# Kernel tuning notes

Measured on AMD Instinct MI355X. Metric: run time of the kernel, lower is better.

Reference implementation:

```python
import jax, jax.numpy as jnp
import numpy as np
from jax import lax

NODATA_VALUE = 0.0
RADIUS = 16  # structuring element size = 2*RADIUS + 1 = 33


def setup_inputs() -> dict:
    key = jax.random.key(0)
    # binary-ish raster: ~half pixels equal the nodata value (0.0)
    x = jax.random.randint(key, (8, 2048, 2048, 1), 0, 2).astype(jnp.float32)
    return {"x": x}


def reference(x):
    # nodata mask: 1 where x == nodata, else 0 (uint8 in original; float here for reduce_window)
    mask = jnp.where(jnp.equal(x, NODATA_VALUE), 1.0, 0.0).astype(x.dtype)
    se = 1 + 2 * RADIUS
    # tf.nn.dilation2d with an all-zeros kernel == sliding-window max over (se x se),
    # SAME padding. A square max window is separable: row-max then column-max.
    m = lax.reduce_window(mask, -jnp.inf, lax.max,
                          window_dimensions=(1, se, 1, 1),
                          window_strides=(1, 1, 1, 1),
                          padding="SAME")
    m = lax.reduce_window(m, -jnp.inf, lax.max,
                          window_dimensions=(1, 1, se, 1),
                          window_strides=(1, 1, 1, 1),
                          padding="SAME")
    return m.astype(jnp.uint8)
```

## Files before the change

### kernel.cpp

```cpp
#include <hip/hip_runtime.h>
#include <stdint.h>


#define HH_ 2048
#define WW_PX 2048
#define WW 32
#define RAD 16
#define ROWS 16
#define TPB2 512

typedef float  vfloat4 __attribute__((ext_vector_type(4)));
typedef int    vint4   __attribute__((ext_vector_type(4)));

__device__ __forceinline__ uint64_t spread4(uint64_t x) {
  x &= 0xFFFFULL;
  x = (x | (x << 24)) & 0x000000FF000000FFULL;
  x = (x | (x << 12)) & 0x000F000F000F000FULL;
  x = (x | (x << 6))  & 0x0303030303030303ULL;
  x = (x | (x << 3))  & 0x1111111111111111ULL;
  return x;
}

__global__ __launch_bounds__(256) void pack_kernel(const float* __restrict__ x,
                                                   uint64_t* __restrict__ packed) {
  const long long px0 = ((long long)blockIdx.x * 256 + threadIdx.x) * 4;
  const vfloat4 v = __builtin_nontemporal_load((const vfloat4*)(x + px0));
  const unsigned long long m0 = __ballot(v.x == 0.0f);
  const unsigned long long m1 = __ballot(v.y == 0.0f);
  const unsigned long long m2 = __ballot(v.z == 0.0f);
  const unsigned long long m3 = __ballot(v.w == 0.0f);
  const int lane = threadIdx.x & 63;
  if ((lane & 15) == 0) {
    const int sh = lane;
    uint64_t w = spread4(m0 >> sh)
               | (spread4(m1 >> sh) << 1)
               | (spread4(m2 >> sh) << 2)
               | (spread4(m3 >> sh) << 3);
    packed[px0 >> 6] = w;
  }
}

__global__ __launch_bounds__(TPB2) void dilate_kernel(const uint64_t* __restrict__ packed,
                                                      int* __restrict__ out) {
  __shared__ uint64_t stage[ROWS + 2 * RAD][WW];
  __shared__ uint64_t vall[ROWS][WW + 2];
  __shared__ uint64_t hrow[ROWS][WW];

  const int t = threadIdx.x;
  const int gr0 = blockIdx.x * ROWS;
  const int n = gr0 >> 11;
  const int h0 = gr0 & 2047;
  const uint64_t* base = packed + (long long)n * (HH_ * WW);

#pragma unroll
  for (int i = 0; i < (ROWS + 2 * RAD) * WW / TPB2; ++i) {
    const int idx = i * TPB2 + t;
    const int rr = idx >> 5;
    const int w_ = idx & 31;
    int hh = h0 + rr - RAD;
    hh = hh < 0 ? 0 : (hh > HH_ - 1 ? HH_ - 1 : hh);
    stage[rr][w_] = base[hh * WW + w_];
  }
  __syncthreads();

  const int w = t & 31;
  const int r = t >> 5;
  uint64_t v = 0;
#pragma unroll
  for (int i = 0; i <= 2 * RAD; ++i) v |= stage[r + i][w];
  vall[r][w + 1] = v;
  if (w == 0) { vall[r][0] = 0; vall[r][WW + 1] = 0; }
  __syncthreads();

  {
    const uint64_t p = vall[r][w];
    const uint64_t c = vall[r][w + 1];
    const uint64_t nx = vall[r][w + 2];
    uint64_t res = c;
#pragma unroll
    for (int s = 1; s <= RAD; ++s) {
      res |= (c >> s) | (nx << (64 - s));
      res |= (c << s) | (p >> (64 - s));
    }
    hrow[r][w] = res;
  }
  __syncthreads();

  int* obase = out + (long long)gr0 * WW_PX;
#pragma unroll
  for (int it = 0; it < 16; ++it) {
    const int f = it * TPB2 + t;
    const int row_l = f >> 9;
    const int wi = (f >> 4) & 31;
    const int sh = (f & 15) * 4;
    const uint64_t bits = hrow[row_l][wi] >> sh;
    vint4 o;
    o.x = (int)(bits & 1);
    o.y = (int)((bits >> 1) & 1);
    o.z = (int)((bits >> 2) & 1);
    o.w = (int)((bits >> 3) & 1);
    __builtin_nontemporal_store(o, (vint4*)(obase + (long long)f * 4));
  }
}

extern "C" void kernel_launch(void* const* d_in, const int* in_sizes, int n_in,
                              void* d_out, int out_size, void* d_ws, size_t ws_size,
                              hipStream_t stream) {
  const float* x = (const float*)d_in[0];
  int* out = (int*)d_out;
  uint64_t* packed = (uint64_t*)d_ws;

  hipLaunchKernelGGL(pack_kernel, dim3(32768), dim3(256), 0, stream, x, packed);
  hipLaunchKernelGGL(dilate_kernel, dim3(1024), dim3(TPB2), 0, stream, packed, out);
}
```

Measured before the change: 224.7 us.

## Fuse mask packing into dilation kernel and enlarge row tiles

Removes the separate pack kernel and its workspace round-trip. Each block now reads float rows directly and ballots them into bitmasks in shared memory. The tile height doubles to 32 rows so the 32-row halo re-read is amortized (64 rows read per 32 output). Block indices are swizzled across images. The cost is that halo input rows are re-read as full float32 data rather than packed bits, and there are fewer blocks (512).

New measurement: 248.9 us. 1.11x slower.

```diff
diff --git a/kernel.cpp b/kernel.cpp
--- a/kernel.cpp
+++ b/kernel.cpp
@@ -2,15 +2,16 @@
 #include <stdint.h>
 
 
-#define HH_ 2048
-#define WW_PX 2048
+#define HH 2048
+#define WPX 2048
 #define WW 32
 #define RAD 16
-#define ROWS 16
-#define TPB2 512
+#define ROWS 32
+#define SROWS (ROWS + 2 * RAD)
+#define TPB 512
 
-typedef float  vfloat4 __attribute__((ext_vector_type(4)));
-typedef int    vint4   __attribute__((ext_vector_type(4)));
+typedef float vfloat4 __attribute__((ext_vector_type(4)));
+typedef int   vint4   __attribute__((ext_vector_type(4)));
 
 __device__ __forceinline__ uint64_t spread4(uint64_t x) {
   x &= 0xFFFFULL;
@@ -21,75 +22,75 @@
   return x;
 }
 
-__global__ __launch_bounds__(256) void pack_kernel(const float* __restrict__ x,
-                                                   uint64_t* __restrict__ packed) {
-  const long long px0 = ((long long)blockIdx.x * 256 + threadIdx.x) * 4;
-  const vfloat4 v = __builtin_nontemporal_load((const vfloat4*)(x + px0));
-  const unsigned long long m0 = __ballot(v.x == 0.0f);
-  const unsigned long long m1 = __ballot(v.y == 0.0f);
-  const unsigned long long m2 = __ballot(v.z == 0.0f);
-  const unsigned long long m3 = __ballot(v.w == 0.0f);
-  const int lane = threadIdx.x & 63;
-  if ((lane & 15) == 0) {
-    const int sh = lane;
-    uint64_t w = spread4(m0 >> sh)
-               | (spread4(m1 >> sh) << 1)
-               | (spread4(m2 >> sh) << 2)
-               | (spread4(m3 >> sh) << 3);
-    packed[px0 >> 6] = w;
-  }
-}
-
-__global__ __launch_bounds__(TPB2) void dilate_kernel(const uint64_t* __restrict__ packed,
-                                                      int* __restrict__ out) {
-  __shared__ uint64_t stage[ROWS + 2 * RAD][WW];
+__global__ __launch_bounds__(TPB) void fused_dilate_kernel(const float* __restrict__ x,
+                                                           int* __restrict__ out) {
+  __shared__ uint64_t stage[SROWS][WW];
   __shared__ uint64_t vall[ROWS][WW + 2];
   __shared__ uint64_t hrow[ROWS][WW];
 
+  const int cpx = gridDim.x >> 3;
+  const int tile = (blockIdx.x & 7) * cpx + (blockIdx.x >> 3);
+  const int gr0 = tile * ROWS;
+  const int n  = gr0 >> 11;
+  const int h0 = gr0 & (HH - 1);
+  const float* xb = x + (long long)n * HH * WPX;
+
   const int t = threadIdx.x;
-  const int gr0 = blockIdx.x * ROWS;
-  const int n = gr0 >> 11;
-  const int h0 = gr0 & 2047;
-  const uint64_t* base = packed + (long long)n * (HH_ * WW);
+  const int lane = t & 63;
+  const int wv = t >> 6;
 
-#pragma unroll
-  for (int i = 0; i < (ROWS + 2 * RAD) * WW / TPB2; ++i) {
-    const int idx = i * TPB2 + t;
-    const int rr = idx >> 5;
-    const int w_ = idx & 31;
+#pragma unroll 8
+  for (int rr = 0; rr < SROWS; ++rr) {
     int hh = h0 + rr - RAD;
-    hh = hh < 0 ? 0 : (hh > HH_ - 1 ? HH_ - 1 : hh);
-    stage[rr][w_] = base[hh * WW + w_];
+    hh = hh < 0 ? 0 : (hh > HH - 1 ? HH - 1 : hh);
+    const vfloat4 v = *(const vfloat4*)(xb + (long long)hh * WPX + (t << 2));
+    const unsigned long long m0 = __ballot(v.x == 0.0f);
+    const unsigned long long m1 = __ballot(v.y == 0.0f);
+    const unsigned long long m2 = __ballot(v.z == 0.0f);
+    const unsigned long long m3 = __ballot(v.w == 0.0f);
+    if ((lane & 15) == 0) {
+      const int sh = lane;
+      stage[rr][(wv << 2) + (lane >> 4)] =
+          spread4(m0 >> sh) | (spread4(m1 >> sh) << 1) |
+          (spread4(m2 >> sh) << 2) | (spread4(m3 >> sh) << 3);
+    }
   }
   __syncthreads();
 
   const int w = t & 31;
   const int r = t >> 5;
-  uint64_t v = 0;
+
 #pragma unroll
-  for (int i = 0; i <= 2 * RAD; ++i) v |= stage[r + i][w];
-  vall[r][w + 1] = v;
-  if (w == 0) { vall[r][0] = 0; vall[r][WW + 1] = 0; }
+  for (int rb = 0; rb < ROWS / 16; ++rb) {
+    const int rr = r + rb * 16;
+    uint64_t v = 0;
+#pragma unroll
+    for (int i = 0; i <= 2 * RAD; ++i) v |= stage[rr + i][w];
+    vall[rr][w + 1] = v;
+    if (w == 0) { vall[rr][0] = 0; vall[rr][WW + 1] = 0; }
+  }
   __syncthreads();
 
-  {
-    const uint64_t p = vall[r][w];
-    const uint64_t c = vall[r][w + 1];
-    const uint64_t nx = vall[r][w + 2];
+#pragma unroll
+  for (int rb = 0; rb < ROWS / 16; ++rb) {
+    const int rr = r + rb * 16;
+    const uint64_t p  = vall[rr][w];
+    const uint64_t c  = vall[rr][w + 1];
+    const uint64_t nx = vall[rr][w + 2];
     uint64_t res = c;
 #pragma unroll
     for (int s = 1; s <= RAD; ++s) {
       res |= (c >> s) | (nx << (64 - s));
       res |= (c << s) | (p >> (64 - s));
     }
-    hrow[r][w] = res;
+    hrow[rr][w] = res;
   }
   __syncthreads();
 
-  int* obase = out + (long long)gr0 * WW_PX;
+  int* obase = out + (long long)gr0 * WPX;
 #pragma unroll
-  for (int it = 0; it < 16; ++it) {
-    const int f = it * TPB2 + t;
+  for (int it = 0; it < ROWS * (WPX / 4) / TPB; ++it) {
+    const int f = it * TPB + t;
     const int row_l = f >> 9;
     const int wi = (f >> 4) & 31;
     const int sh = (f & 15) * 4;
@@ -108,8 +109,5 @@
                               hipStream_t stream) {
   const float* x = (const float*)d_in[0];
   int* out = (int*)d_out;
-  uint64_t* packed = (uint64_t*)d_ws;
-
-  hipLaunchKernelGGL(pack_kernel, dim3(32768), dim3(256), 0, stream, x, packed);
-  hipLaunchKernelGGL(dilate_kernel, dim3(1024), dim3(TPB2), 0, stream, packed, out);
+  hipLaunchKernelGGL(fused_dilate_kernel, dim3(512), dim3(TPB), 0, stream, x, out);
 }
```
